# Kernel tuning notes

Measured on AMD Instinct MI355X. Metric: run time of the kernel, lower is better.

Reference implementation:

```python
import math
import jax, jax.numpy as jnp
import numpy as np
from jax import lax

B, IMG, CIN, ED, TD, M = 32, 224, 3, 64, 64, 32
DILATIONS = (1, 2, 3, 4)
KS, STRIDE = 7, 4


def _conv2d(x, w, b, stride, pad, dil=1):
    y = lax.conv_general_dilated(x, w, (stride, stride), [(pad, pad), (pad, pad)],
                                 rhs_dilation=(dil, dil),
                                 dimension_numbers=('NCHW', 'OIHW', 'NCHW'))
    return y + b[None, :, None, None]


def _ln(x, g, b):
    mu = x.mean(-1, keepdims=True)
    var = ((x - mu) ** 2).mean(-1, keepdims=True)
    return (x - mu) / jnp.sqrt(var + 1e-5) * g + b


def setup_inputs() -> dict:
    key = jax.random.key(0)
    ks = jax.random.split(key, 25)
    s = 0.05
    rn = lambda k, shp: (jax.random.normal(k, shp) * s).astype(jnp.float32)
    inp = {}
    inp['x'] = jax.random.normal(ks[0], (B, CIN, IMG, IMG), dtype=jnp.float32)
    # PRM dilated conv weights (stacked over 4 dilations)
    inp['prm_w'] = rn(ks[1], (4, ED, CIN, KS, KS))
    inp['prm_b'] = rn(ks[2], (4, ED))
    # PCM stem: conv-SiLU, conv-BN-SiLU, conv-SiLU
    inp['pcm_w1'] = rn(ks[3], (ED, CIN, 3, 3))
    inp['pcm_b1'] = rn(ks[4], (ED,))
    inp['pcm_w2'] = rn(ks[5], (ED, ED, 3, 3))
    inp['pcm_b2'] = rn(ks[6], (ED,))
    inp['bn_g'] = 1.0 + rn(ks[7], (ED,))
    inp['bn_b'] = rn(ks[8], (ED,))
    inp['bn_mean'] = rn(ks[9], (ED,))
    inp['bn_var'] = jax.random.uniform(ks[10], (ED,), minval=0.5, maxval=1.5).astype(jnp.float32)
    inp['pcm_w3'] = rn(ks[11], (TD, ED, 3, 3))
    inp['pcm_b3'] = rn(ks[12], (TD,))
    # Token_performer params (dim = 4*ED = 256, emb = TD = 64, m = 32)
    dim = 4 * ED
    inp['ln1_g'] = 1.0 + rn(ks[13], (dim,))
    inp['ln1_b'] = rn(ks[14], (dim,))
    inp['kqv_w'] = rn(ks[15], (3 * TD, dim))
    inp['kqv_b'] = rn(ks[16], (3 * TD,))
    # orthogonal random-feature matrix, rows orthonormal, scaled by sqrt(m)
    a = np.random.default_rng(0).normal(size=(TD, TD))
    qmat, _ = np.linalg.qr(a)
    inp['w_perf'] = jnp.asarray(qmat[:M] * math.sqrt(M), dtype=jnp.float32)
    inp['proj_w'] = rn(ks[17], (TD, TD))
    inp['proj_b'] = rn(ks[18], (TD,))
    inp['ln2_g'] = 1.0 + rn(ks[19], (TD,))
    inp['ln2_b'] = rn(ks[20], (TD,))
    inp['mlp_w1'] = rn(ks[21], (TD, TD))
    inp['mlp_b1'] = rn(ks[22], (TD,))
    inp['mlp_w2'] = rn(ks[23], (TD, TD))
    inp['mlp_b2'] = rn(ks[24], (TD,))
    inp['H'] = IMG
    inp['W'] = IMG
    return inp


def reference(x, prm_w, prm_b, pcm_w1, pcm_b1, pcm_w2, pcm_b2, bn_g, bn_b, bn_mean,
              bn_var, pcm_w3, pcm_b3, ln1_g, ln1_b, kqv_w, kqv_b, w_perf, proj_w,
              proj_b, ln2_g, ln2_b, mlp_w1, mlp_b1, mlp_w2, mlp_b2, H, W):
    Bx = x.shape[0]
    Hp, Wp = H // STRIDE, W // STRIDE
    # --- PRM: parallel dilated Conv2d + GELU branches ---
    branches = []
    for i, d in enumerate(DILATIONS):  # fixed small set of structurally distinct convs
        pad = math.ceil(((KS - 1) * d + 1 - STRIDE) / 2)
        branches.append(jax.nn.gelu(_conv2d(x, prm_w[i], prm_b[i], STRIDE, pad, d),
                                    approximate=False))
    y = jnp.stack(branches, axis=1)  # [B, 4, ED, Hp, Wp]
    prm_x = y.reshape(Bx, len(DILATIONS) * ED, Hp * Wp).transpose(0, 2, 1)  # [B, N, 256]
    # --- PCM stem: conv-SiLU / conv-BN-SiLU / conv-SiLU (eval-mode BN) ---
    c = jax.nn.silu(_conv2d(x, pcm_w1, pcm_b1, 2, 1))
    c = _conv2d(c, pcm_w2, pcm_b2, 2, 1)
    inv = (bn_g / jnp.sqrt(bn_var + 1e-5))[None, :, None, None]
    c = (c - bn_mean[None, :, None, None]) * inv + bn_b[None, :, None, None]
    c = jax.nn.silu(c)
    c = jax.nn.silu(_conv2d(c, pcm_w3, pcm_b3, 1, 1))  # [B, TD, Hp, Wp]
    convX = c.transpose(0, 2, 3, 1).reshape(Bx, Hp * Wp, TD)
    # --- Performer kernelized attention ---
    xn = _ln(prm_x, ln1_g, ln1_b)
    kqv = xn @ kqv_w.T + kqv_b
    k, q, v = kqv[..., :TD], kqv[..., TD:2 * TD], kqv[..., 2 * TD:]

    def prm_exp(z):
        xd = 0.5 * (z * z).sum(-1, keepdims=True)          # [B, N, 1]
        wtx = jnp.einsum('bti,mi->btm', z, w_perf)          # [B, N, M]
        return jnp.exp(wtx - xd) / math.sqrt(M)

    kp, qp = prm_exp(k), prm_exp(q)                         # [B, N, M]
    D = jnp.einsum('btm,bm->bt', qp, kp.sum(axis=1))[..., None]  # [B, N, 1]
    kptv = jnp.einsum('btn,btm->bnm', v, kp)                # [B, TD, M]
    ya = jnp.einsum('btm,bnm->btn', qp, kptv) / (D + 1e-8)  # [B, N, TD]
    ya = v + ya @ proj_w.T + proj_b
    # --- combine + MLP block ---
    xo = ya + convX
    h = _ln(xo, ln2_g, ln2_b)
    h = jax.nn.gelu(h @ mlp_w1.T + mlp_b1, approximate=False) @ mlp_w2.T + mlp_b2
    return xo + h
```

## Files before the change

kernel.cpp:

```cpp
#include <hip/hip_runtime.h>
#include <hip/hip_bf16.h>
#include <cstddef>

#define BB    32
#define IMG   224
#define CIN   3
#define ED    64
#define TD    64
#define MM    32
#define HP    56
#define TT    3136
#define C4    256
#define KQVN  192

typedef __attribute__((ext_vector_type(8))) short bf16x8;
typedef __attribute__((ext_vector_type(4))) float f32x4;

#define OFF_CONVX  0u
#define OFF_XN     6422528u
#define OFF_C2B    6422528u
#define OFF_C1B    19267584u
#define OFF_V      19267584u
#define OFF_KP     25690112u
#define OFF_QP     28901376u
#define OFF_PART   32112640u
#define OFF_KPTV   33161216u
#define OFF_KPSP   (OFF_KPTV + 32768u)
#define OFF_KPSUM  33226752u
#define OFF_WPT    (OFF_PART)
#define OFF_WKB    (OFF_PART + 37632u)
#define OFF_WC2B   (OFF_PART + 62208u)
#define OFF_WT3B   (OFF_PART + 80640u)
#define OFF_WC1B   (OFF_PART + 99072u)

__device__ __forceinline__ float geluf(float v){
  return 0.5f*v*(1.f + erff(v*0.70710678118654752f));
}
__device__ __forceinline__ float siluf(float v){
  return v/(1.f + expf(-v));
}
__device__ __forceinline__ ushort bfbits(float v){
  __hip_bfloat16 h = __float2bfloat16(v);
  return *reinterpret_cast<ushort*>(&h);
}

__global__ __launch_bounds__(256) void k_wtrans(
    const float* __restrict__ prm_w, const float* __restrict__ kqv_w,
    const float* __restrict__ pcm_w2, const float* __restrict__ pcm_w3,
    const float* __restrict__ pcm_w1,
    float* __restrict__ wpt, __hip_bfloat16* __restrict__ wkb,
    __hip_bfloat16* __restrict__ wc2b, __hip_bfloat16* __restrict__ wt3b,
    __hip_bfloat16* __restrict__ wc1b)
{
  int idx = blockIdx.x*256 + threadIdx.x;
  if (idx < 37632){
    int oc = idx & 63, r = idx >> 6;
    int i = r/147, tap = r - i*147;
    wpt[idx] = prm_w[(i*64 + oc)*147 + tap];
  } else if (idx < 86784){
    int i4 = idx - 37632;
    wkb[i4] = __float2bfloat16(kqv_w[i4]);
  } else if (idx < 123648){
    int i2 = idx - 86784;
    int oc = i2/576, rem = i2 - oc*576;
    int khkw = rem >> 6, ci = rem & 63;
    int kh = khkw/3, kw = khkw - kh*3;
    wc2b[i2] = __float2bfloat16(pcm_w2[(oc*64+ci)*9 + kh*3 + kw]);
  } else if (idx < 160512){
    int i3 = idx - 123648;
    int oc = i3/576, rem = i3 - oc*576;
    int khkw = rem >> 6, ci = rem & 63;
    int kh = khkw/3, kw = khkw - kh*3;
    wt3b[i3] = __float2bfloat16(pcm_w3[(oc*64+ci)*9 + kh*3 + kw]);
  } else if (idx < 162560){
    int i5 = idx - 160512;
    int oc = i5 >> 5, k = i5 & 31;
    float v = 0.f;
    if (k < 27) v = pcm_w1[oc*27 + k];
    wc1b[i5] = __float2bfloat16(v);
  }
}

__global__ __launch_bounds__(256) void k_conv1(
    const float* __restrict__ x, const __hip_bfloat16* __restrict__ wc1b,
    const float* __restrict__ bias, __hip_bfloat16* __restrict__ c1b)
{
  __shared__ __align__(16) ushort xs[3*17*18];
  __shared__ __align__(16) ushort As[64*40];
  const int t = threadIdx.x;
  const int b = blockIdx.y;
  const int th = blockIdx.x/14, tw = blockIdx.x - th*14;
  const int oh0 = th*8, ow0 = tw*8;
  const int ih0 = oh0*2 - 1, iw0 = ow0*2 - 1;
  const int w = t>>6, lane = t&63, l15 = lane&15, hi = lane>>4;

  const float* xb = x + (size_t)b*CIN*IMG*IMG;
  for (int idx = t; idx < 918; idx += 256){
    int ci = idx/306, rem = idx - ci*306;
    int r = rem/18, c = rem - r*18;
    float v = 0.f;
    int ih = ih0 + r, iw = iw0 + c;
    if (c < 17 && (unsigned)ih < 224u && (unsigned)iw < 224u)
      v = xb[(ci*IMG+ih)*IMG+iw];
    xs[idx] = bfbits(v);
  }
  __syncthreads();
  for (int idx = t; idx < 2048; idx += 256){
    int pos = idx >> 5, k = idx & 31;
    ushort v = 0;
    if (k < 27){
      int ci = k/9, rem = k - ci*9;
      int kh = rem/3, kw = rem - kh*3;
      v = xs[(ci*17 + (pos>>3)*2 + kh)*18 + (pos&7)*2 + kw];
    }
    As[pos*40 + k] = v;
  }
  __syncthreads();

  float bs4[4];
  #pragma unroll
  for (int nb=0;nb<4;++nb) bs4[nb] = bias[nb*16+l15];
  f32x4 acc[4];
  #pragma unroll
  for (int nb=0;nb<4;++nb) acc[nb] = (f32x4){0.f,0.f,0.f,0.f};
  const ushort* wq = (const ushort*)wc1b;
  {
    bf16x8 a = *(const bf16x8*)&As[(w*16+l15)*40 + hi*8];
    #pragma unroll
    for (int nb=0;nb<4;++nb){
      bf16x8 bv = *(const bf16x8*)&wq[(nb*16+l15)*32 + hi*8];
      acc[nb] = __builtin_amdgcn_mfma_f32_16x16x32_bf16(a, bv, acc[nb], 0, 0, 0);
    }
  }
  #pragma unroll
  for (int nb=0;nb<4;++nb){
    #pragma unroll
    for (int r=0;r<4;++r){
      int row = w*16 + hi*4 + r;
      int oh = oh0 + (row>>3), ow = ow0 + (row&7);
      c1b[(((size_t)b*112+oh)*112+ow)*64 + nb*16+l15] =
        __float2bfloat16(siluf(acc[nb][r] + bs4[nb]));
    }
  }
}

__global__ __launch_bounds__(256) void k_conv2(
    const __hip_bfloat16* __restrict__ c1b, const __hip_bfloat16* __restrict__ wc2b,
    const float* __restrict__ bias, const float* __restrict__ g,
    const float* __restrict__ bb, const float* __restrict__ mean,
    const float* __restrict__ var, __hip_bfloat16* __restrict__ c2b)
{
  __shared__ __align__(16) ushort xs[17*17*72];
  const int b = blockIdx.y;
  const int th = blockIdx.x/7, tw = blockIdx.x - th*7;
  const int oh0 = th*8, ow0 = tw*8;
  const int t = threadIdx.x;
  const int w = t>>6, lane = t&63, l15 = lane&15, hi = lane>>4;

  const int ih0 = oh0*2-1, iw0 = ow0*2-1;
  const ushort* c1u = (const ushort*)c1b;
  for (int seg = t; seg < 2312; seg += 256){
    int pos = seg >> 3, s8 = seg & 7;
    int r = pos/17, c = pos - r*17;
    int ih = ih0 + r, iw = iw0 + c;
    uint4 val = {0,0,0,0};
    if ((unsigned)ih < 112u && (unsigned)iw < 112u)
      val = *(const uint4*)&c1u[(((size_t)b*112+ih)*112+iw)*64 + s8*8];
    *(uint4*)&xs[(r*17+c)*72 + s8*8] = val;
  }
  __syncthreads();

  float bs4[4], iv4[4], mn4[4], bo4[4];
  #pragma unroll
  for (int nb=0;nb<4;++nb){
    int oc = nb*16+l15;
    bs4[nb] = bias[oc];
    iv4[nb] = g[oc]*rsqrtf(var[oc]+1e-5f);
    mn4[nb] = mean[oc];
    bo4[nb] = bb[oc];
  }

  f32x4 acc[4];
  #pragma unroll
  for (int nb=0;nb<4;++nb) acc[nb] = (f32x4){0.f,0.f,0.f,0.f};

  const int p = w*16 + l15, pr = p>>3, pc = p&7;
  const ushort* wq = (const ushort*)wc2b;

  for (int ks=0; ks<18; ++ks){
    const int k0 = ks*32 + hi*8;
    const int khkw = k0 >> 6, ci0 = k0 & 63;
    const int kh = khkw/3, kw = khkw - kh*3;
    bf16x8 a = *(const bf16x8*)&xs[((2*pr+kh)*17 + 2*pc+kw)*72 + ci0];
    #pragma unroll
    for (int nb=0;nb<4;++nb){
      bf16x8 bv = *(const bf16x8*)&wq[(nb*16+l15)*576 + k0];
      acc[nb] = __builtin_amdgcn_mfma_f32_16x16x32_bf16(a, bv, acc[nb], 0, 0, 0);
    }
  }

  #pragma unroll
  for (int nb=0;nb<4;++nb){
    #pragma unroll
    for (int r=0;r<4;++r){
      int pp = w*16 + hi*4 + r;
      int oh = oh0 + (pp>>3), ow = ow0 + (pp&7);
      float vv = acc[nb][r] + bs4[nb];
      vv = (vv - mn4[nb])*iv4[nb] + bo4[nb];
      c2b[(((size_t)b*56+oh)*56+ow)*64 + nb*16+l15] = __float2bfloat16(siluf(vv));
    }
  }
}

__global__ __launch_bounds__(256) void k_conv3(
    const __hip_bfloat16* __restrict__ c2b, const __hip_bfloat16* __restrict__ wt3b,
    const float* __restrict__ bias, float* __restrict__ convX)
{
  __shared__ __align__(16) ushort xs[10*12*72];
  const int b = blockIdx.y;
  const int th = blockIdx.x/7, tw = blockIdx.x - th*7;
  const int oh0 = th*8, ow0 = tw*8;
  const int t = threadIdx.x;
  const int w = t>>6, lane = t&63, l15 = lane&15, hi = lane>>4;

  const ushort* c2u = (const ushort*)c2b;
  for (int seg = t; seg < 960; seg += 256){
    int pos = seg >> 3, s8 = seg & 7;
    int r = pos/12, c = pos - r*12;
    int ih = oh0 - 1 + r, iw = ow0 - 1 + c;
    uint4 val = {0,0,0,0};
    if ((unsigned)ih < 56u && (unsigned)iw < 56u)
      val = *(const uint4*)&c2u[(((size_t)b*56+ih)*56+iw)*64 + s8*8];
    *(uint4*)&xs[(r*12+c)*72 + s8*8] = val;
  }
  __syncthreads();

  float bs4[4];
  #pragma unroll
  for (int nb=0;nb<4;++nb) bs4[nb] = bias[nb*16+l15];

  f32x4 acc[4];
  #pragma unroll
  for (int nb=0;nb<4;++nb) acc[nb] = (f32x4){0.f,0.f,0.f,0.f};

  const int p = w*16 + l15, pr = p>>3, pc = p&7;
  const ushort* wq = (const ushort*)wt3b;

  for (int ks=0; ks<18; ++ks){
    const int k0 = ks*32 + hi*8;
    const int khkw = k0 >> 6, ci0 = k0 & 63;
    const int kh = khkw/3, kw = khkw - kh*3;
    bf16x8 a = *(const bf16x8*)&xs[((pr+kh)*12 + pc+kw)*72 + ci0];
    #pragma unroll
    for (int nb=0;nb<4;++nb){
      bf16x8 bv = *(const bf16x8*)&wq[(nb*16+l15)*576 + k0];
      acc[nb] = __builtin_amdgcn_mfma_f32_16x16x32_bf16(a, bv, acc[nb], 0, 0, 0);
    }
  }

  #pragma unroll
  for (int nb=0;nb<4;++nb){
    #pragma unroll
    for (int r=0;r<4;++r){
      int pp = w*16 + hi*4 + r;
      int oh = oh0 + (pp>>3), ow = ow0 + (pp&7);
      int s = oh*HP + ow;
      convX[((size_t)b*TT + s)*64 + nb*16+l15] = siluf(acc[nb][r] + bs4[nb]);
    }
  }
}

#define LOADX(PH) do{ const float4* xr_ = (const float4*)(rowb + (PH)*20); \
  *(float4*)&X[0]=xr_[0]; *(float4*)&X[4]=xr_[1]; *(float4*)&X[8]=xr_[2]; \
  *(float4*)&X[12]=xr_[3]; *(float4*)&X[16]=xr_[4]; }while(0)
#define TAP(KW,Q0) do{ const float wv_ = wrow[(KW)*64]; \
  v[0]+=wv_*X[(Q0)+0];  v[1]+=wv_*X[(Q0)+1];  v[2]+=wv_*X[(Q0)+2];  v[3]+=wv_*X[(Q0)+3]; \
  v[4]+=wv_*X[(Q0)+4];  v[5]+=wv_*X[(Q0)+5];  v[6]+=wv_*X[(Q0)+6];  v[7]+=wv_*X[(Q0)+7]; \
  v[8]+=wv_*X[(Q0)+8];  v[9]+=wv_*X[(Q0)+9];  v[10]+=wv_*X[(Q0)+10]; v[11]+=wv_*X[(Q0)+11]; \
  v[12]+=wv_*X[(Q0)+12]; v[13]+=wv_*X[(Q0)+13]; }while(0)

template<int D>
__device__ __forceinline__ void prm_core(const float* __restrict__ xt2,
    const float* __restrict__ wq, float v[14])
{
  constexpr int R0 = 12 - 3*D;
  #pragma unroll 1
  for (int ci=0; ci<3; ++ci){
    #pragma unroll 1
    for (int kh=0; kh<7; ++kh){
      const float* rowb = xt2 + ci*2000 + (R0 + kh*D)*80;
      const float* wrow = wq + ((ci*7+kh)*7)*64;
      float X[20];
      if constexpr (D == 1){
        LOADX(0); TAP(3,3);
        LOADX(1); TAP(0,2); TAP(4,3);
        LOADX(2); TAP(1,2); TAP(5,3);
        LOADX(3); TAP(2,2); TAP(6,3);
      } else if constexpr (D == 2){
        LOADX(0); TAP(1,2); TAP(3,3); TAP(5,4);
        LOADX(2); TAP(0,1); TAP(2,2); TAP(4,3); TAP(6,4);
      } else if constexpr (D == 3){
        LOADX(0); TAP(3,3);
        LOADX(1); TAP(2,2); TAP(6,5);
        LOADX(2); TAP(1,1); TAP(5,4);
        LOADX(3); TAP(0,0); TAP(4,3);
      } else {
        LOADX(0); TAP(0,0); TAP(1,1); TAP(2,2); TAP(3,3); TAP(4,4); TAP(5,5); TAP(6,6);
      }
    }
  }
}

__global__ __launch_bounds__(256) void k_prm_ln(
    const float* __restrict__ x, const float* __restrict__ wpt,
    const float* __restrict__ prm_b, const float* __restrict__ ln_g,
    const float* __restrict__ ln_b, __hip_bfloat16* __restrict__ xn, int b0)
{
  __shared__ __align__(16) float xt2[6000];
  __shared__ float wred[4][14][2];
  const int t = threadIdx.x;
  const int b = blockIdx.y + b0;
  const int oh  = blockIdx.x >> 2;
  const int owt = blockIdx.x & 3;
  const int ow0 = owt*14;
  const int ih0 = oh*4 - 11;
  const int iw0 = ow0*4 - 11;

  const float* xb = x + (size_t)b*CIN*IMG*IMG;
  for (int idx = t; idx < 6000; idx += 256){
    int ci  = idx / 2000;
    int rem = idx - ci*2000;
    int r   = rem / 80;
    int cc  = rem - r*80;
    int ih = ih0 + r, iw = iw0 + cc;
    float val = 0.f;
    if ((unsigned)ih < (unsigned)IMG && (unsigned)iw < (unsigned)IMG)
      val = xb[(ci*IMG+ih)*IMG+iw];
    xt2[(ci*25 + r)*80 + (cc&3)*20 + (cc>>2)] = val;
  }
  __syncthreads();

  const int i = t >> 6, lane = t & 63;
  float v[14];
  const float bi = prm_b[i*64+lane];
  #pragma unroll
  for (int p=0;p<14;++p) v[p] = bi;
  const float* wq = wpt + (i*147)*64 + lane;

  if      (i == 0) prm_core<1>(xt2, wq, v);
  else if (i == 1) prm_core<2>(xt2, wq, v);
  else if (i == 2) prm_core<3>(xt2, wq, v);
  else             prm_core<4>(xt2, wq, v);

  #pragma unroll
  for (int p=0;p<14;++p) v[p] = geluf(v[p]);
  #pragma unroll
  for (int p=0;p<14;++p){
    float s1 = v[p], s2 = v[p]*v[p];
    #pragma unroll
    for (int o=32;o;o>>=1){
      s1 += __shfl_xor(s1, o, 64);
      s2 += __shfl_xor(s2, o, 64);
    }
    if (lane == 0){ wred[i][p][0] = s1; wred[i][p][1] = s2; }
  }
  __syncthreads();
  const float lg = ln_g[t], lb = ln_b[t];
  const int s_base = oh*HP + ow0;
  #pragma unroll
  for (int p=0;p<14;++p){
    float S1 = wred[0][p][0]+wred[1][p][0]+wred[2][p][0]+wred[3][p][0];
    float S2 = wred[0][p][1]+wred[1][p][1]+wred[2][p][1]+wred[3][p][1];
    float mu = S1*(1.f/256.f);
    float rs = rsqrtf(S2*(1.f/256.f) - mu*mu + 1e-5f);
    float outv = (v[p]-mu)*rs*lg + lb;
    xn[((size_t)(b*TT + s_base + p))*256 + t] = __float2bfloat16(outv);
  }
}

__global__ __launch_bounds__(256) void k_kqv_perf(
    const __hip_bfloat16* __restrict__ xn, const __hip_bfloat16* __restrict__ wkb,
    const float* __restrict__ kqv_b, const float* __restrict__ wperf,
    float* __restrict__ v_g, float* __restrict__ kp, float* __restrict__ qp)
{
  __shared__ __align__(16) char smem[36864];
  __shared__ float wperf_s[32*68];
  __shared__ float kqvb_s[192];
  __shared__ float xd_s[128];
  ushort* As = (ushort*)smem;
  ushort* Bs = (ushort*)(smem + 9216);
  float*  zq = (float*)smem;

  const int t = threadIdx.x;
  const int m0 = blockIdx.x*64;
  const int w = t >> 6, lane = t & 63;
  const int l15 = lane & 15, hi = lane >> 4;

  for (int idx = t; idx < 2048; idx += 256)
    wperf_s[(idx>>6)*68 + (idx&63)] = wperf[idx];
  if (t < 192) kqvb_s[t] = kqv_b[t];

  f32x4 acc[12];
  #pragma unroll
  for (int nb=0;nb<12;++nb) acc[nb] = (f32x4){0.f,0.f,0.f,0.f};

  const ushort* xnu = (const ushort*)xn;
  const ushort* wku = (const ushort*)wkb;

  for (int kc=0; kc<4; ++kc){
    #pragma unroll
    for (int ss=0; ss<2; ++ss){
      int seg = ss*256 + t;
      int row = seg >> 3, c8 = seg & 7;
      *(uint4*)&As[row*72 + c8*8] =
        *(const uint4*)&xnu[((size_t)(m0+row))*256 + kc*64 + c8*8];
    }
    #pragma unroll
    for (int ss=0; ss<6; ++ss){
      int seg = ss*256 + t;
      int row = seg >> 3, c8 = seg & 7;
      *(uint4*)&Bs[row*72 + c8*8] =
        *(const uint4*)&wku[row*256 + kc*64 + c8*8];
    }
    __syncthreads();
    #pragma unroll
    for (int ks=0; ks<2; ++ks){
      bf16x8 a = *(const bf16x8*)&As[(16*w + l15)*72 + ks*32 + hi*8];
      #pragma unroll
      for (int nb=0;nb<12;++nb){
        bf16x8 bv = *(const bf16x8*)&Bs[(nb*16 + l15)*72 + ks*32 + hi*8];
        acc[nb] = __builtin_amdgcn_mfma_f32_16x16x32_bf16(a, bv, acc[nb], 0, 0, 0);
      }
    }
    __syncthreads();
  }

  #pragma unroll
  for (int nb=0;nb<12;++nb){
    int col = nb*16 + l15;
    float bias = kqvb_s[col];
    #pragma unroll
    for (int r=0;r<4;++r){
      int row = w*16 + hi*4 + r;
      float val = acc[nb][r] + bias;
      if (col < 128) zq[row*132 + col] = val;
      else v_g[((size_t)(m0+row))*64 + (col-128)] = val;
    }
  }
  __syncthreads();

  if (t < 128){
    int pos = t & 63, wh = t >> 6;
    const float4* zr4 = (const float4*)&zq[pos*132 + wh*64];
    float s = 0.f;
    #pragma unroll
    for (int c4=0;c4<16;++c4){
      float4 z4 = zr4[c4];
      s += z4.x*z4.x + z4.y*z4.y + z4.z*z4.z + z4.w*z4.w;
    }
    xd_s[t] = 0.5f*s;
  }
  __syncthreads();

  {
    const int qi = t >> 1, mbase = (t & 1)*16;
    const int pos = qi & 63, wh = qi >> 6;
    const float4* zr4 = (const float4*)&zq[pos*132 + wh*64];
    float wtx[16];
    #pragma unroll
    for (int j=0;j<16;++j) wtx[j] = 0.f;
    #pragma unroll 4
    for (int c4=0;c4<16;++c4){
      float4 z4 = zr4[c4];
      #pragma unroll
      for (int j=0;j<16;++j){
        const float4 w4 = *(const float4*)&wperf_s[(mbase+j)*68 + c4*4];
        wtx[j] += z4.x*w4.x + z4.y*w4.y + z4.z*w4.z + z4.w*w4.w;
      }
    }
    const float xd = xd_s[qi];
    float* dst = wh ? qp : kp;
    float* dp = dst + ((size_t)(m0+pos))*32 + mbase;
    #pragma unroll
    for (int j4=0;j4<4;++j4){
      float4 o;
      o.x = expf(wtx[j4*4+0] - xd) * 0.17677669529663687f;
      o.y = expf(wtx[j4*4+1] - xd) * 0.17677669529663687f;
      o.z = expf(wtx[j4*4+2] - xd) * 0.17677669529663687f;
      o.w = expf(wtx[j4*4+3] - xd) * 0.17677669529663687f;
      *(float4*)&dp[j4*4] = o;
    }
  }
}

__global__ __launch_bounds__(256) void k_kptv(
    const float* __restrict__ v_g, const float* __restrict__ kp,
    float* __restrict__ part, float* __restrict__ kpsum_part)
{
  const int b = blockIdx.y, g = blockIdx.x;
  const int n = threadIdx.x & 63, mg = threadIdx.x >> 6;
  float acc[8] = {0,0,0,0,0,0,0,0};
  float ksum[8] = {0,0,0,0,0,0,0,0};
  for (int tt = g*196; tt < (g+1)*196; ++tt){
    float vv = v_g[((size_t)b*TT + tt)*64 + n];
    const float4* kp4 = (const float4*)(kp + ((size_t)b*TT + tt)*MM + mg*8);
    float4 a0 = kp4[0], a1 = kp4[1];
    acc[0] += vv*a0.x; acc[1] += vv*a0.y; acc[2] += vv*a0.z; acc[3] += vv*a0.w;
    acc[4] += vv*a1.x; acc[5] += vv*a1.y; acc[6] += vv*a1.z; acc[7] += vv*a1.w;
    if (n == 0){
      ksum[0]+=a0.x; ksum[1]+=a0.y; ksum[2]+=a0.z; ksum[3]+=a0.w;
      ksum[4]+=a1.x; ksum[5]+=a1.y; ksum[6]+=a1.z; ksum[7]+=a1.w;
    }
  }
  #pragma unroll
  for (int j=0;j<8;++j)
    part[(((size_t)g*BB + b)*64 + n)*MM + mg*8 + j] = acc[j];
  if (n == 0){
    #pragma unroll
    for (int j=0;j<8;++j)
      kpsum_part[(size_t)g*1024 + b*32 + mg*8 + j] = ksum[j];
  }
}

__global__ __launch_bounds__(256) void k_kptv_red(
    const float* __restrict__ part, const float* __restrict__ kpsum_part,
    __hip_bfloat16* __restrict__ kptvb, float* __restrict__ kpsum)
{
  const int t = threadIdx.x;
  const int idx = blockIdx.x*256 + t;
  float a = 0.f;
  #pragma unroll
  for (int g=0; g<16; ++g) a += part[(size_t)g*65536 + idx];
  kptvb[idx] = __float2bfloat16(a);
  if (blockIdx.x < 4){
    int kidx = blockIdx.x*256 + t;
    float s = 0.f;
    #pragma unroll
    for (int g=0; g<16; ++g) s += kpsum_part[(size_t)g*1024 + kidx];
    kpsum[kidx] = s;
  }
}

__global__ __launch_bounds__(256) void k_attn_mlp(
    const float* __restrict__ v_g, const float* __restrict__ qp,
    const float* __restrict__ kpsum, const __hip_bfloat16* __restrict__ kptvb,
    const float* __restrict__ projw, const float* __restrict__ projb,
    const float* __restrict__ convX,
    const float* __restrict__ ln2_g, const float* __restrict__ ln2_b,
    const float* __restrict__ w1, const float* __restrict__ b1,
    const float* __restrict__ w2, const float* __restrict__ b2,
    float* __restrict__ out)
{
  __shared__ __align__(16) char smem[64512];
  ushort* qpb = (ushort*)smem;
  ushort* ktb = (ushort*)(smem + 5120);
  ushort* pjw = (ushort*)(smem + 10240);
  ushort* hb  = (ushort*)smem;
  ushort* t2  = (ushort*)(smem + 19456);
  ushort* w1b = (ushort*)(smem + 28672);
  ushort* w2b = (ushort*)(smem + 37888);
  float*  xosh= (float*)(smem + 47104);
  __shared__ float Ds[64];
  __shared__ float Dp[4][64];
  __shared__ float ks_s[32], pjb_s[64], b1_s[64], b2_s[64], g2_s[64], bb2_s[64];

  const int t = threadIdx.x;
  const int b = blockIdx.y;
  const int p0 = blockIdx.x*64;
  const int w = t>>6, lane = t&63, l15 = lane&15, hi = lane>>4;

  const float* qpg = qp + ((size_t)b*TT + p0)*32;
  for (int idx = t; idx < 2048; idx += 256)
    qpb[(idx>>5)*40 + (idx&31)] = bfbits(qpg[idx]);
  const ushort* ktg = (const ushort*)kptvb + (size_t)b*2048;
  for (int idx = t; idx < 2048; idx += 256)
    ktb[(idx>>5)*40 + (idx&31)] = ktg[idx];
  for (int idx = t; idx < 4096; idx += 256){
    pjw[(idx>>6)*72 + (idx&63)] = bfbits(projw[idx]);
    w1b[(idx>>6)*72 + (idx&63)] = bfbits(w1[idx]);
    w2b[(idx>>6)*72 + (idx&63)] = bfbits(w2[idx]);
  }
  if (t < 32) ks_s[t] = kpsum[b*MM + t];
  if (t < 64){
    pjb_s[t] = projb[t]; b1_s[t] = b1[t]; b2_s[t] = b2[t];
    g2_s[t] = ln2_g[t];  bb2_s[t] = ln2_b[t];
  }
  __syncthreads();

  {
    int pos = t & 63, grp = t >> 6;
    float s = 0.f;
    #pragma unroll
    for (int j=0;j<8;++j){
      int m = grp*8 + j;
      __hip_bfloat16 h = *reinterpret_cast<__hip_bfloat16*>(&qpb[pos*40 + m]);
      s += __bfloat162float(h) * ks_s[m];
    }
    Dp[grp][pos] = s;
  }
  __syncthreads();
  if (t < 64) Ds[t] = Dp[0][t]+Dp[1][t]+Dp[2][t]+Dp[3][t] + 1e-8f;
  __syncthreads();

  f32x4 acc1[4];
  #pragma unroll
  for (int nb=0;nb<4;++nb) acc1[nb] = (f32x4){0.f,0.f,0.f,0.f};
  {
    bf16x8 a = *(const bf16x8*)&qpb[(w*16 + l15)*40 + hi*8];
    #pragma unroll
    for (int nb=0;nb<4;++nb){
      bf16x8 bv = *(const bf16x8*)&ktb[(nb*16 + l15)*40 + hi*8];
      acc1[nb] = __builtin_amdgcn_mfma_f32_16x16x32_bf16(a, bv, acc1[nb], 0, 0, 0);
    }
  }
  #pragma unroll
  for (int nb=0;nb<4;++nb){
    #pragma unroll
    for (int r=0;r<4;++r){
      int row = w*16 + hi*4 + r;
      t2[row*72 + nb*16 + l15] = bfbits(acc1[nb][r] / Ds[row]);
    }
  }
  __syncthreads();

  f32x4 acc2[4];
  #pragma unroll
  for (int nb=0;nb<4;++nb) acc2[nb] = (f32x4){0.f,0.f,0.f,0.f};
  #pragma unroll
  for (int ks=0; ks<2; ++ks){
    bf16x8 a2 = *(const bf16x8*)&t2[(w*16 + l15)*72 + ks*32 + hi*8];
    #pragma unroll
    for (int nb=0;nb<4;++nb){
      bf16x8 bv2 = *(const bf16x8*)&pjw[(nb*16 + l15)*72 + ks*32 + hi*8];
      acc2[nb] = __builtin_amdgcn_mfma_f32_16x16x32_bf16(a2, bv2, acc2[nb], 0, 0, 0);
    }
  }
  #pragma unroll
  for (int nb=0;nb<4;++nb){
    #pragma unroll
    for (int r=0;r<4;++r){
      int row = w*16 + hi*4 + r;
      int col = nb*16 + l15;
      const size_t off = ((size_t)b*TT + p0 + row)*64 + col;
      xosh[row*68 + col] = v_g[off] + acc2[nb][r] + pjb_s[col] + convX[off];
    }
  }
  __syncthreads();

  {
    const int n = t & 63, p = t >> 6;
    const float g2 = g2_s[n], bb2 = bb2_s[n];
    for (int sp=0; sp<16; ++sp){
      const int pos = sp*4 + p;
      const float xv = xosh[pos*68 + n];
      float s1 = xv, s2 = xv*xv;
      #pragma unroll
      for (int o=32;o;o>>=1){
        s1 += __shfl_xor(s1, o, 64);
        s2 += __shfl_xor(s2, o, 64);
      }
      float mu = s1*(1.f/64.f);
      float rs = rsqrtf(s2*(1.f/64.f) - mu*mu + 1e-5f);
      t2[pos*72 + n] = bfbits((xv - mu)*rs*g2 + bb2);
    }
  }
  __syncthreads();

  f32x4 acc3[4];
  #pragma unroll
  for (int nb=0;nb<4;++nb) acc3[nb] = (f32x4){0.f,0.f,0.f,0.f};
  #pragma unroll
  for (int ks=0; ks<2; ++ks){
    bf16x8 a3 = *(const bf16x8*)&t2[(w*16 + l15)*72 + ks*32 + hi*8];
    #pragma unroll
    for (int nb=0;nb<4;++nb){
      bf16x8 bv3 = *(const bf16x8*)&w1b[(nb*16 + l15)*72 + ks*32 + hi*8];
      acc3[nb] = __builtin_amdgcn_mfma_f32_16x16x32_bf16(a3, bv3, acc3[nb], 0, 0, 0);
    }
  }
  __syncthreads();
  #pragma unroll
  for (int nb=0;nb<4;++nb){
    #pragma unroll
    for (int r=0;r<4;++r){
      int row = w*16 + hi*4 + r;
      int col = nb*16 + l15;
      hb[row*72 + col] = bfbits(geluf(acc3[nb][r] + b1_s[col]));
    }
  }
  __syncthreads();

  f32x4 acc4[4];
  #pragma unroll
  for (int nb=0;nb<4;++nb) acc4[nb] = (f32x4){0.f,0.f,0.f,0.f};
  #pragma unroll
  for (int ks=0; ks<2; ++ks){
    bf16x8 a4 = *(const bf16x8*)&hb[(w*16 + l15)*72 + ks*32 + hi*8];
    #pragma unroll
    for (int nb=0;nb<4;++nb){
      bf16x8 bv4 = *(const bf16x8*)&w2b[(nb*16 + l15)*72 + ks*32 + hi*8];
      acc4[nb] = __builtin_amdgcn_mfma_f32_16x16x32_bf16(a4, bv4, acc4[nb], 0, 0, 0);
    }
  }
  #pragma unroll
  for (int nb=0;nb<4;++nb){
    #pragma unroll
    for (int r=0;r<4;++r){
      int row = w*16 + hi*4 + r;
      int col = nb*16 + l15;
      const size_t off = ((size_t)b*TT + p0 + row)*64 + col;
      out[off] = xosh[row*68 + col] + acc4[nb][r] + b2_s[col];
    }
  }
}

extern "C" void kernel_launch(void* const* d_in, const int* in_sizes, int n_in,
                              void* d_out, int out_size, void* d_ws, size_t ws_size,
                              hipStream_t stream)
{
  const float* x      = (const float*)d_in[0];
  const float* prm_w  = (const float*)d_in[1];
  const float* prm_b  = (const float*)d_in[2];
  const float* pcm_w1 = (const float*)d_in[3];
  const float* pcm_b1 = (const float*)d_in[4];
  const float* pcm_w2 = (const float*)d_in[5];
  const float* pcm_b2 = (const float*)d_in[6];
  const float* bn_g   = (const float*)d_in[7];
  const float* bn_b   = (const float*)d_in[8];
  const float* bn_mean= (const float*)d_in[9];
  const float* bn_var = (const float*)d_in[10];
  const float* pcm_w3 = (const float*)d_in[11];
  const float* pcm_b3 = (const float*)d_in[12];
  const float* ln1_g  = (const float*)d_in[13];
  const float* ln1_b  = (const float*)d_in[14];
  const float* kqv_w  = (const float*)d_in[15];
  const float* kqv_b  = (const float*)d_in[16];
  const float* w_perf = (const float*)d_in[17];
  const float* proj_w = (const float*)d_in[18];
  const float* proj_b = (const float*)d_in[19];
  const float* ln2_g  = (const float*)d_in[20];
  const float* ln2_b  = (const float*)d_in[21];
  const float* mlp_w1 = (const float*)d_in[22];
  const float* mlp_b1 = (const float*)d_in[23];
  const float* mlp_w2 = (const float*)d_in[24];
  const float* mlp_b2 = (const float*)d_in[25];

  float* ws = (float*)d_ws;
  float* convX = ws + OFF_CONVX;
  __hip_bfloat16* xn  = (__hip_bfloat16*)(ws + OFF_XN);
  __hip_bfloat16* c2b = (__hip_bfloat16*)(ws + OFF_C2B);
  __hip_bfloat16* c1b = (__hip_bfloat16*)(ws + OFF_C1B);
  float* v_g   = ws + OFF_V;
  float* kp    = ws + OFF_KP;
  float* qp    = ws + OFF_QP;
  float* part  = ws + OFF_PART;
  __hip_bfloat16* kptvb = (__hip_bfloat16*)(ws + OFF_KPTV);
  float* kpsum_part = ws + OFF_KPSP;
  float* kpsum = ws + OFF_KPSUM;
  float* wpt   = ws + OFF_WPT;
  __hip_bfloat16* wkb  = (__hip_bfloat16*)(ws + OFF_WKB);
  __hip_bfloat16* wc2b = (__hip_bfloat16*)(ws + OFF_WC2B);
  __hip_bfloat16* wt3b = (__hip_bfloat16*)(ws + OFF_WT3B);
  __hip_bfloat16* wc1b = (__hip_bfloat16*)(ws + OFF_WC1B);
  float* out   = (float*)d_out;

  k_wtrans<<<dim3(636), 256, 0, stream>>>(prm_w, kqv_w, pcm_w2, pcm_w3, pcm_w1,
                                          wpt, wkb, wc2b, wt3b, wc1b);
  k_conv1<<<dim3(196,BB), 256, 0, stream>>>(x, wc1b, pcm_b1, c1b);
  k_conv2<<<dim3(49,BB), 256, 0, stream>>>(c1b, wc2b, pcm_b2, bn_g, bn_b,
                                           bn_mean, bn_var, c2b);
  k_conv3<<<dim3(49,BB), 256, 0, stream>>>(c2b, wt3b, pcm_b3, convX);
  k_prm_ln<<<dim3(224,16), 256, 0, stream>>>(x, wpt, prm_b, ln1_g, ln1_b, xn, 0);
  k_prm_ln<<<dim3(224,16), 256, 0, stream>>>(x, wpt, prm_b, ln1_g, ln1_b, xn, 16);
  k_kqv_perf<<<dim3(1568), 256, 0, stream>>>(xn, wkb, kqv_b, w_perf, v_g, kp, qp);
  k_kptv<<<dim3(16,BB), 256, 0, stream>>>(v_g, kp, part, kpsum_part);
  k_kptv_red<<<dim3(256), 256, 0, stream>>>(part, kpsum_part, kptvb, kpsum);
  k_attn_mlp<<<dim3(49,BB), 256, 0, stream>>>(v_g, qp, kpsum, kptvb, proj_w, proj_b,
                                              convX, ln2_g, ln2_b, mlp_w1, mlp_b1,
                                              mlp_w2, mlp_b2, out);
}
```

Measured before the change: 560.0 us.

## Use MFMA for kptv reduction, pre-convert MLP weights, merge prm_ln launches

Rewrites the k_kptv reduction (v^T·kp over token chunks) to stage transposed bf16 tiles in shared memory and compute them with 16x16x32 bf16 MFMA, replacing the scalar fp32 per-thread FMA loop. The kp column sums are now taken from the staged bf16 values in shared memory. Projection and MLP weights are converted to bf16 once in k_wtrans, so each k_attn_mlp block no longer converts fp32 weights itself. The two half-batch k_prm_ln launches become one full-batch launch. The cost is lower precision, since v, kp and the kp sums are now rounded to bf16.

```diff
diff --git a/kernel.cpp b/kernel.cpp
--- a/kernel.cpp
+++ b/kernel.cpp
@@ -26,6 +26,9 @@
 #define OFF_PART   32112640u
 #define OFF_KPTV   33161216u
 #define OFF_KPSP   (OFF_KPTV + 32768u)
+#define OFF_WPJB   (OFF_KPTV + 49152u)
+#define OFF_WM1B   (OFF_KPTV + 51200u)
+#define OFF_WM2B   (OFF_KPTV + 53248u)
 #define OFF_KPSUM  33226752u
 #define OFF_WPT    (OFF_PART)
 #define OFF_WKB    (OFF_PART + 37632u)
@@ -47,10 +50,12 @@
 __global__ __launch_bounds__(256) void k_wtrans(
     const float* __restrict__ prm_w, const float* __restrict__ kqv_w,
     const float* __restrict__ pcm_w2, const float* __restrict__ pcm_w3,
-    const float* __restrict__ pcm_w1,
+    const float* __restrict__ pcm_w1, const float* __restrict__ proj_w,
+    const float* __restrict__ mlp_w1, const float* __restrict__ mlp_w2,
     float* __restrict__ wpt, __hip_bfloat16* __restrict__ wkb,
     __hip_bfloat16* __restrict__ wc2b, __hip_bfloat16* __restrict__ wt3b,
-    __hip_bfloat16* __restrict__ wc1b)
+    __hip_bfloat16* __restrict__ wc1b, __hip_bfloat16* __restrict__ wpjb,
+    __hip_bfloat16* __restrict__ wm1b, __hip_bfloat16* __restrict__ wm2b)
 {
   int idx = blockIdx.x*256 + threadIdx.x;
   if (idx < 37632){
@@ -78,6 +83,12 @@
     float v = 0.f;
     if (k < 27) v = pcm_w1[oc*27 + k];
     wc1b[i5] = __float2bfloat16(v);
+  } else if (idx < 166656){
+    wpjb[idx - 162560] = __float2bfloat16(proj_w[idx - 162560]);
+  } else if (idx < 170752){
+    wm1b[idx - 166656] = __float2bfloat16(mlp_w1[idx - 166656]);
+  } else if (idx < 174848){
+    wm2b[idx - 170752] = __float2bfloat16(mlp_w2[idx - 170752]);
   }
 }
 
@@ -314,12 +325,12 @@
 __global__ __launch_bounds__(256) void k_prm_ln(
     const float* __restrict__ x, const float* __restrict__ wpt,
     const float* __restrict__ prm_b, const float* __restrict__ ln_g,
-    const float* __restrict__ ln_b, __hip_bfloat16* __restrict__ xn, int b0)
+    const float* __restrict__ ln_b, __hip_bfloat16* __restrict__ xn)
 {
   __shared__ __align__(16) float xt2[6000];
   __shared__ float wred[4][14][2];
   const int t = threadIdx.x;
-  const int b = blockIdx.y + b0;
+  const int b = blockIdx.y;
   const int oh  = blockIdx.x >> 2;
   const int owt = blockIdx.x & 3;
   const int ow0 = owt*14;
@@ -497,28 +508,63 @@
     const float* __restrict__ v_g, const float* __restrict__ kp,
     float* __restrict__ part, float* __restrict__ kpsum_part)
 {
+  __shared__ __align__(16) ushort vT[64*232];
+  __shared__ __align__(16) ushort kpT[32*232];
+  __shared__ float ksh[8][32];
   const int b = blockIdx.y, g = blockIdx.x;
-  const int n = threadIdx.x & 63, mg = threadIdx.x >> 6;
-  float acc[8] = {0,0,0,0,0,0,0,0};
-  float ksum[8] = {0,0,0,0,0,0,0,0};
-  for (int tt = g*196; tt < (g+1)*196; ++tt){
-    float vv = v_g[((size_t)b*TT + tt)*64 + n];
-    const float4* kp4 = (const float4*)(kp + ((size_t)b*TT + tt)*MM + mg*8);
-    float4 a0 = kp4[0], a1 = kp4[1];
-    acc[0] += vv*a0.x; acc[1] += vv*a0.y; acc[2] += vv*a0.z; acc[3] += vv*a0.w;
-    acc[4] += vv*a1.x; acc[5] += vv*a1.y; acc[6] += vv*a1.z; acc[7] += vv*a1.w;
-    if (n == 0){
-      ksum[0]+=a0.x; ksum[1]+=a0.y; ksum[2]+=a0.z; ksum[3]+=a0.w;
-      ksum[4]+=a1.x; ksum[5]+=a1.y; ksum[6]+=a1.z; ksum[7]+=a1.w;
-    }
-  }
-  #pragma unroll
-  for (int j=0;j<8;++j)
-    part[(((size_t)g*BB + b)*64 + n)*MM + mg*8 + j] = acc[j];
-  if (n == 0){
-    #pragma unroll
-    for (int j=0;j<8;++j)
-      kpsum_part[(size_t)g*1024 + b*32 + mg*8 + j] = ksum[j];
+  const int t = threadIdx.x;
+  const int w = t>>6, lane = t&63, l15 = lane&15, hi = lane>>4;
+  const int t0 = g*196;
+
+  for (int idx = t; idx < 14336; idx += 256){
+    int tt = idx >> 6, n = idx & 63;
+    float vv = (tt < 196) ? v_g[((size_t)b*TT + t0 + tt)*64 + n] : 0.f;
+    vT[n*232 + tt] = bfbits(vv);
+  }
+  for (int idx = t; idx < 7168; idx += 256){
+    int tt = idx >> 5, m = idx & 31;
+    float kv = (tt < 196) ? kp[((size_t)b*TT + t0 + tt)*32 + m] : 0.f;
+    kpT[m*232 + tt] = bfbits(kv);
+  }
+  __syncthreads();
+
+  f32x4 accp[2];
+  accp[0] = (f32x4){0.f,0.f,0.f,0.f};
+  accp[1] = (f32x4){0.f,0.f,0.f,0.f};
+  for (int ks=0; ks<7; ++ks){
+    bf16x8 a = *(const bf16x8*)&vT[(w*16+l15)*232 + ks*32 + hi*8];
+    #pragma unroll
+    for (int nt=0; nt<2; ++nt){
+      bf16x8 bv = *(const bf16x8*)&kpT[(nt*16+l15)*232 + ks*32 + hi*8];
+      accp[nt] = __builtin_amdgcn_mfma_f32_16x16x32_bf16(a, bv, accp[nt], 0, 0, 0);
+    }
+  }
+  #pragma unroll
+  for (int nt=0;nt<2;++nt){
+    #pragma unroll
+    for (int r=0;r<4;++r){
+      int row = w*16 + hi*4 + r;
+      int col = nt*16 + l15;
+      part[(((size_t)g*BB + b)*64 + row)*MM + col] = accp[nt][r];
+    }
+  }
+  {
+    int m = t & 31, h8 = t >> 5;
+    float s = 0.f;
+    int lo = h8*25, hic = lo+25 < 196 ? lo+25 : 196;
+    for (int tt = lo; tt < hic; ++tt){
+      ushort u = kpT[m*232 + tt];
+      __hip_bfloat16 hv = *reinterpret_cast<__hip_bfloat16*>(&u);
+      s += __bfloat162float(hv);
+    }
+    ksh[h8][m] = s;
+  }
+  __syncthreads();
+  if (t < 32){
+    float s = 0.f;
+    #pragma unroll
+    for (int j=0;j<8;++j) s += ksh[j][t];
+    kpsum_part[(size_t)g*1024 + b*32 + t] = s;
   }
 }
 
@@ -544,11 +590,11 @@
 __global__ __launch_bounds__(256) void k_attn_mlp(
     const float* __restrict__ v_g, const float* __restrict__ qp,
     const float* __restrict__ kpsum, const __hip_bfloat16* __restrict__ kptvb,
-    const float* __restrict__ projw, const float* __restrict__ projb,
+    const __hip_bfloat16* __restrict__ wpjb, const float* __restrict__ projb,
     const float* __restrict__ convX,
     const float* __restrict__ ln2_g, const float* __restrict__ ln2_b,
-    const float* __restrict__ w1, const float* __restrict__ b1,
-    const float* __restrict__ w2, const float* __restrict__ b2,
+    const __hip_bfloat16* __restrict__ wm1b, const float* __restrict__ b1,
+    const __hip_bfloat16* __restrict__ wm2b, const float* __restrict__ b2,
     float* __restrict__ out)
 {
   __shared__ __align__(16) char smem[64512];
@@ -575,10 +621,13 @@
   const ushort* ktg = (const ushort*)kptvb + (size_t)b*2048;
   for (int idx = t; idx < 2048; idx += 256)
     ktb[(idx>>5)*40 + (idx&31)] = ktg[idx];
+  const ushort* pju = (const ushort*)wpjb;
+  const ushort* w1u = (const ushort*)wm1b;
+  const ushort* w2u = (const ushort*)wm2b;
   for (int idx = t; idx < 4096; idx += 256){
-    pjw[(idx>>6)*72 + (idx&63)] = bfbits(projw[idx]);
-    w1b[(idx>>6)*72 + (idx&63)] = bfbits(w1[idx]);
-    w2b[(idx>>6)*72 + (idx&63)] = bfbits(w2[idx]);
+    pjw[(idx>>6)*72 + (idx&63)] = pju[idx];
+    w1b[(idx>>6)*72 + (idx&63)] = w1u[idx];
+    w2b[(idx>>6)*72 + (idx&63)] = w2u[idx];
   }
   if (t < 32) ks_s[t] = kpsum[b*MM + t];
   if (t < 64){
@@ -762,20 +811,24 @@
   __hip_bfloat16* wc2b = (__hip_bfloat16*)(ws + OFF_WC2B);
   __hip_bfloat16* wt3b = (__hip_bfloat16*)(ws + OFF_WT3B);
   __hip_bfloat16* wc1b = (__hip_bfloat16*)(ws + OFF_WC1B);
+  __hip_bfloat16* wpjb = (__hip_bfloat16*)(ws + OFF_WPJB);
+  __hip_bfloat16* wm1b = (__hip_bfloat16*)(ws + OFF_WM1B);
+  __hip_bfloat16* wm2b = (__hip_bfloat16*)(ws + OFF_WM2B);
   float* out   = (float*)d_out;
 
-  k_wtrans<<<dim3(636), 256, 0, stream>>>(prm_w, kqv_w, pcm_w2, pcm_w3, pcm_w1,
-                                          wpt, wkb, wc2b, wt3b, wc1b);
+  k_wtrans<<<dim3(683), 256, 0, stream>>>(prm_w, kqv_w, pcm_w2, pcm_w3, pcm_w1,
+                                          proj_w, mlp_w1, mlp_w2,
+                                          wpt, wkb, wc2b, wt3b, wc1b,
+                                          wpjb, wm1b, wm2b);
   k_conv1<<<dim3(196,BB), 256, 0, stream>>>(x, wc1b, pcm_b1, c1b);
   k_conv2<<<dim3(49,BB), 256, 0, stream>>>(c1b, wc2b, pcm_b2, bn_g, bn_b,
                                            bn_mean, bn_var, c2b);
   k_conv3<<<dim3(49,BB), 256, 0, stream>>>(c2b, wt3b, pcm_b3, convX);
-  k_prm_ln<<<dim3(224,16), 256, 0, stream>>>(x, wpt, prm_b, ln1_g, ln1_b, xn, 0);
-  k_prm_ln<<<dim3(224,16), 256, 0, stream>>>(x, wpt, prm_b, ln1_g, ln1_b, xn, 16);
+  k_prm_ln<<<dim3(224,BB), 256, 0, stream>>>(x, wpt, prm_b, ln1_g, ln1_b, xn);
   k_kqv_perf<<<dim3(1568), 256, 0, stream>>>(xn, wkb, kqv_b, w_perf, v_g, kp, qp);
   k_kptv<<<dim3(16,BB), 256, 0, stream>>>(v_g, kp, part, kpsum_part);
   k_kptv_red<<<dim3(256), 256, 0, stream>>>(part, kpsum_part, kptvb, kpsum);
-  k_attn_mlp<<<dim3(49,BB), 256, 0, stream>>>(v_g, qp, kpsum, kptvb, proj_w, proj_b,
-                                              convX, ln2_g, ln2_b, mlp_w1, mlp_b1,
-                                              mlp_w2, mlp_b2, out);
-}
+  k_attn_mlp<<<dim3(49,BB), 256, 0, stream>>>(v_g, qp, kpsum, kptvb, wpjb, proj_b,
+                                              convX, ln2_g, ln2_b, wm1b, mlp_b1,
+                                              wm2b, mlp_b2, out);
+}
```

Result: faster. 494.8 us (-11.7%).
